# Kernel optimization log

Hardware: AMD Instinct MI355X
Metric: run time of the kernel (lower is better)

Reference implementation:

```python
import jax, jax.numpy as jnp
import numpy as np

D, L, G, B, T = 512, 2, 64, 64, 512  # n_dim, n_layers, n_gaussian, batch, seq_len


def lstm_cell(x, h, c, Wih, Whh, bih, bhh):
    # PyTorch gate order: input, forget, cell(g), output
    g = x @ Wih.T + bih + h @ Whh.T + bhh  # [B, 4D]
    i, f, gg, o = jnp.split(g, 4, axis=-1)
    c = jax.nn.sigmoid(f) * c + jax.nn.sigmoid(i) * jnp.tanh(gg)
    h = jax.nn.sigmoid(o) * jnp.tanh(c)
    return h, c


def encode(x, Wih, Whh, bih, bhh):
    n = x.shape[0]
    xt = jnp.transpose(x, (1, 0, 2))  # [T, B, D]
    hs, cs = [], []
    for l in range(L):
        def step(carry, xv, l=l):
            h, c = carry
            h, c = lstm_cell(xv, h, c, Wih[l], Whh[l], bih[l], bhh[l])
            return (h, c), h
        z = jnp.zeros((n, D), x.dtype)
        (hT, cT), xt = jax.lax.scan(step, (z, z), xt)
        hs.append(hT); cs.append(cT)
    return jnp.stack(hs), jnp.stack(cs)  # [L, B, D] each


def decode(prev0, h0, c0, Wih, Whh, bih, bhh, length):
    def step(carry, _):
        prev, h, c = carry
        x = prev
        nh, nc = [], []
        for l in range(L):
            hl, cl = lstm_cell(x, h[l], c[l], Wih[l], Whh[l], bih[l], bhh[l])
            nh.append(hl); nc.append(cl); x = hl
        return (x, jnp.stack(nh), jnp.stack(nc)), x
    _, ys = jax.lax.scan(step, (prev0, h0, c0), None, length=length)
    return jnp.transpose(ys, (1, 0, 2))  # [B, T, D]


def vae(h, muW, mub, sigW, sigb, outW, outb, eps):
    mu = jnp.einsum('lbd,lgd->lbg', h, muW) + mub[:, None, :]
    sig = jnp.einsum('lbd,lgd->lbg', h, sigW) + sigb[:, None, :]
    z = mu + eps * sig  # reparameterization
    out = jnp.einsum('lbg,ldg->lbd', z, outW) + outb[:, None, :]
    return out, mu, sig


def setup_inputs() -> dict:
    key = jax.random.key(0)
    ks = jax.random.split(key, 26)
    kk = 1.0 / np.sqrt(D)
    u = lambda i, shp: jax.random.uniform(ks[i], shp, jnp.float32, -kk, kk)
    return {
        "x": jax.random.normal(ks[0], (B, T, D), jnp.float32),
        "initial": jnp.zeros((1, D), jnp.float32),
        "enc_Wih": u(1, (L, 4 * D, D)), "enc_Whh": u(2, (L, 4 * D, D)),
        "enc_bih": u(3, (L, 4 * D)), "enc_bhh": u(4, (L, 4 * D)),
        "dec_Wih": u(5, (L, 4 * D, D)), "dec_Whh": u(6, (L, 4 * D, D)),
        "dec_bih": u(7, (L, 4 * D)), "dec_bhh": u(8, (L, 4 * D)),
        "h_mu_W": u(9, (L, G, D)), "h_mu_b": u(10, (L, G)),
        "h_sig_W": u(11, (L, G, D)), "h_sig_b": u(12, (L, G)),
        "h_out_W": u(13, (L, D, G)), "h_out_b": u(14, (L, D)),
        "c_mu_W": u(15, (L, G, D)), "c_mu_b": u(16, (L, G)),
        "c_sig_W": u(17, (L, G, D)), "c_sig_b": u(18, (L, G)),
        "c_out_W": u(19, (L, D, G)), "c_out_b": u(20, (L, D)),
        "eps_h": jax.random.normal(ks[21], (L, B, G), jnp.float32),
        "eps_c": jax.random.normal(ks[22], (L, B, G), jnp.float32),
    }


def reference(x, initial, enc_Wih, enc_Whh, enc_bih, enc_bhh,
              dec_Wih, dec_Whh, dec_bih, dec_bhh,
              h_mu_W, h_mu_b, h_sig_W, h_sig_b, h_out_W, h_out_b,
              c_mu_W, c_mu_b, c_sig_W, c_sig_b, c_out_W, c_out_b,
              eps_h, eps_c):
    h, c = encode(x, enc_Wih, enc_Whh, enc_bih, enc_bhh)
    h2, hmu, hsig = vae(h, h_mu_W, h_mu_b, h_sig_W, h_sig_b, h_out_W, h_out_b, eps_h)
    c2, cmu, csig = vae(c, c_mu_W, c_mu_b, c_sig_W, c_sig_b, c_out_W, c_out_b, eps_c)
    prev0 = jnp.broadcast_to(initial, (x.shape[0], D))
    out = decode(prev0, h2, c2, dec_Wih, dec_Whh, dec_bih, dec_bhh, x.shape[1])
    return out, jnp.concatenate([hmu, cmu], 0), jnp.concatenate([hsig, csig], 0)
```

## Files before the change

### kernel.cpp

```cpp
#include <hip/hip_runtime.h>
#include <hip/hip_bf16.h>

typedef __bf16 bf16_t;
typedef __attribute__((ext_vector_type(8))) __bf16 bf16x8;
typedef __attribute__((ext_vector_type(4))) float f32x4;
typedef __attribute__((ext_vector_type(4))) int i32x4;

#define MFMA16(a, b, c) __builtin_amdgcn_mfma_f32_16x16x32_bf16((a), (b), (c), 0, 0, 0)

namespace {
constexpr int TSEQ = 512, DDIM = 512, NB = 64;
constexpr size_t OFF_ENC_HBUF = 0;
constexpr size_t OFF_DEC_HBUF = 262144;
constexpr size_t OFF_DEC_YBUF = 524288;
constexpr size_t OFF_HT       = 655360;
constexpr size_t OFF_CT       = 917504;
constexpr size_t OFF_H2       = 1179648;
constexpr size_t OFF_C2       = 1441792;
constexpr size_t OFF_GX       = 2097152;
constexpr size_t GX_BYTES     = (size_t)512 * 256 * 256 * 4;
constexpr int RETRY_CAP = 1 << 14;
template <int V> struct IC { static constexpr int v = V; };
}

__device__ __forceinline__ float sigm_f(float x) { return 1.f / (1.f + __expf(-x)); }
__device__ __forceinline__ float tanh_f(float x) {
  x = fminf(15.f, fmaxf(-15.f, x));
  const float e = __expf(-2.f * x);
  return (1.f - e) / (1.f + e);
}
__device__ __forceinline__ bf16x8 cvt8(const float* __restrict__ p) {
  const float4 a = *(const float4*)p;
  const float4 b = *(const float4*)(p + 4);
  bf16x8 r;
  r[0] = (bf16_t)a.x; r[1] = (bf16_t)a.y; r[2] = (bf16_t)a.z; r[3] = (bf16_t)a.w;
  r[4] = (bf16_t)b.x; r[5] = (bf16_t)b.y; r[6] = (bf16_t)b.z; r[7] = (bf16_t)b.w;
  return r;
}

union FRAG { i32x4 i; bf16x8 v; };

__device__ __forceinline__ unsigned tagpat(int g) {
  return ((((g + 1) >> 1) & 1) ^ 1) ? 0x00010001u : 0u;
}
__device__ __forceinline__ unsigned chk4(const i32x4& v, unsigned pat) {
  unsigned bad = 0;
#pragma unroll
  for (int j = 0; j < 4; ++j) bad |= ((unsigned)v[j] ^ pat) & 0x00010001u;
  return bad;
}

__device__ __forceinline__ void ldg_issue(const bf16_t* p, i32x4& d) {
  asm volatile("global_load_dwordx4 %0, %1, off sc1" : "=v"(d) : "v"(p) : "memory");
}
__device__ __forceinline__ void vm_wait0() {
  asm volatile("s_waitcnt vmcnt(0)" ::: "memory");
  __builtin_amdgcn_sched_barrier(0);
}
__device__ __forceinline__ void stg_tag(bf16_t* p, float a, float b, unsigned pat) {
  union { bf16_t h[2]; unsigned u; } x;
  x.h[0] = (bf16_t)a; x.h[1] = (bf16_t)b;
  __hip_atomic_store((unsigned*)p, (x.u & ~0x00010001u) | pat,
                     __ATOMIC_RELAXED, __HIP_MEMORY_SCOPE_AGENT);
}

__device__ __forceinline__ void load_weights(const float* Wih, const float* Whh,
                                             int wave, int c15, int kg, int d0,
                                             bf16x8 (&wA)[2][8], bf16x8 (&wB)[2][8]) {
  const float* Wsrc = (wave < 2) ? Wih : Whh;
  const int kb = (wave & 1) << 8;
#pragma unroll
  for (int l = 0; l < 2; ++l)
#pragma unroll
    for (int nt = 0; nt < 2; ++nt)
#pragma unroll
      for (int ks = 0; ks < 8; ++ks) {
        const int n = nt * 16 + c15;
        const int grow = (n >> 3) * DDIM + d0 + (n & 7);
        const float* p = Wsrc + (size_t)(l * 2048 + grow) * DDIM + kb + ks * 32 + kg * 8;
        if (nt == 0) wA[l][ks] = cvt8(p);
        else         wB[l][ks] = cvt8(p);
      }
}

__global__ __launch_bounds__(256, 4) void gx_pass(
    const float* __restrict__ x, const float* __restrict__ Wih,
    unsigned* __restrict__ gx) {
  const int wg0 = blockIdx.x & 255;
  const int tc  = blockIdx.x >> 8;
  const int grp = wg0 >> 6, slc = wg0 & 63;
  const int tid = threadIdx.x;
  const int wave = tid >> 6, lane = tid & 63;
  const int c15 = lane & 15, kg = lane >> 4;
  const int b0 = grp << 4, d0 = slc << 3;
  const int kb = (wave & 1) << 8;
  const int tpar = wave >> 1;

  __shared__ float gbuf[2][2][16][33];

  bf16x8 wA[8], wB[8];
#pragma unroll
  for (int nt = 0; nt < 2; ++nt)
#pragma unroll
    for (int ks = 0; ks < 8; ++ks) {
      const int n = nt * 16 + c15;
      const int grow = (n >> 3) * DDIM + d0 + (n & 7);
      const float* p = Wih + (size_t)grow * DDIM + kb + ks * 32 + kg * 8;
      if (nt == 0) wA[ks] = cvt8(p);
      else         wB[ks] = cvt8(p);
    }

  const int b = b0 + c15;
  for (int j = 0; j < 32; ++j) {
    const int t = tc * 64 + 2 * j + tpar;
    f32x4 a0 = {0.f, 0.f, 0.f, 0.f}, a1 = {0.f, 0.f, 0.f, 0.f};
    const float* ap = x + ((size_t)b * TSEQ + t) * DDIM + kb + kg * 8;
#pragma unroll
    for (int ks = 0; ks < 8; ++ks) {
      const bf16x8 a = cvt8(ap + ks * 32);
      a0 = MFMA16(a, wA[ks], a0);
      a1 = MFMA16(a, wB[ks], a1);
    }
#pragma unroll
    for (int r = 0; r < 4; ++r) {
      gbuf[tpar][wave & 1][kg * 4 + r][c15] = a0[r];
      gbuf[tpar][wave & 1][kg * 4 + r][16 + c15] = a1[r];
    }
    __syncthreads();
    if (tid < 128) {
      const int ll = tid >> 6, r6 = tid & 63, rw = r6 >> 2, dp = r6 & 3;
      const int tt = tc * 64 + 2 * j + ll;
      const size_t base = ((size_t)tt * 256 + wg0) * 256 + rw * 16 + dp;
#pragma unroll
      for (int g = 0; g < 4; ++g) {
        const int e = g * 8 + 2 * dp;
        const float v0 = gbuf[ll][0][rw][e] + gbuf[ll][1][rw][e];
        const float v1 = gbuf[ll][0][rw][e + 1] + gbuf[ll][1][rw][e + 1];
        union { _Float16 h[2]; unsigned u; } pk;
        pk.h[0] = (_Float16)v0; pk.h[1] = (_Float16)v1;
        __builtin_nontemporal_store(pk.u, &gx[base + g * 4]);
      }
    }
    __syncthreads();
  }
}

template <int GX>
__global__ __launch_bounds__(256, 1) void enc_pass(
    const float* __restrict__ x,
    const float* __restrict__ Wih, const float* __restrict__ Whh,
    const float* __restrict__ bih, const float* __restrict__ bhh,
    bf16_t* __restrict__ hbuf, float* __restrict__ hT, float* __restrict__ cT,
    const unsigned* __restrict__ gx) {
  const int wg = blockIdx.x;
  const int grp = wg >> 6, slc = wg & 63;
  const int tid = threadIdx.x;
  const int wave = tid >> 6, lane = tid & 63;
  const int b0 = grp << 4, d0 = slc << 3;

  __shared__ float gbuf[2][4][16][33];
  __shared__ float bias_l[2][32];

  const int c15 = lane & 15, kg = lane >> 4;
  const int b = b0 + c15;

  bf16x8 wA[2][8], wB[2][8];
  load_weights(Wih, Whh, wave, c15, kg, d0, wA, wB);
  if (tid < 64) {
    const int l = tid >> 5, n = tid & 31;
    const int grow = (n >> 3) * DDIM + d0 + (n & 7);
    bias_l[l][n] = bih[l * 2048 + grow] + bhh[l * 2048 + grow];
  }
  if (tid < 128) {
    const int l = tid >> 6, r6 = tid & 63, rw = r6 >> 2, dp = r6 & 3;
    const int slot = (l == 0) ? 1 : 0;
    stg_tag(&hbuf[((size_t)(l * 2 + slot) * NB + b0 + rw) * DDIM + d0 + 2 * dp],
            0.f, 0.f, 0x00010001u);
  }
  __syncthreads();

  float cA = 0.f, cB = 0.f;

  for (int s = 0; s <= TSEQ; ++s) {
    const int p = s & 1, rp = p ^ 1;
    const unsigned patold = tagpat(s - 1);
    f32x4 pa0 = {0.f, 0.f, 0.f, 0.f}, pa1 = {0.f, 0.f, 0.f, 0.f};
    unsigned gxr[4];
    if constexpr (GX) {
      if (tid < 64 && s < TSEQ) {
        const size_t base = ((size_t)s * 256 + wg) * 256 + (tid >> 2) * 16 + (tid & 3);
#pragma unroll
        for (int g = 0; g < 4; ++g) gxr[g] = __builtin_nontemporal_load(&gx[base + g * 4]);
      }
    } else {
      if (wave < 2 && s < TSEQ) {
        const int kq = wave << 8;
        const float* ap = x + ((size_t)b * TSEQ + s) * DDIM + kq + kg * 8;
#pragma unroll
        for (int ks = 0; ks < 8; ++ks) {
          const bf16x8 a = cvt8(ap + ks * 32);
          pa0 = MFMA16(a, wA[0][ks], pa0);
          pa1 = MFMA16(a, wB[0][ks], pa1);
        }
      }
    }
    __syncthreads();
    if (wave >= 2) {
      const int kq = (wave - 2) << 8;
      FRAG f0[8], f1[8];
      const bf16_t* a0p = hbuf + ((size_t)(0 * 2 + rp) * NB + b) * DDIM + kq + kg * 8;
      const bf16_t* a1p = hbuf + ((size_t)(1 * 2 + rp) * NB + b) * DDIM + kq + kg * 8;
      int guard = 0;
      for (;;) {
        if (s < TSEQ) {
#pragma unroll
          for (int ks = 0; ks < 8; ++ks) ldg_issue(a0p + ks * 32, f0[ks].i);
        }
        if (s >= 1) {
#pragma unroll
          for (int ks = 0; ks < 8; ++ks) ldg_issue(a1p + ks * 32, f1[ks].i);
        }
        vm_wait0();
        unsigned bad = 0;
        if (s < TSEQ) {
#pragma unroll
          for (int ks = 0; ks < 8; ++ks) bad |= chk4(f0[ks].i, patold);
        }
        if (s >= 1) {
#pragma unroll
          for (int ks = 0; ks < 8; ++ks) bad |= chk4(f1[ks].i, patold);
        }
        if (__all(bad == 0) || ++guard > RETRY_CAP) break;
      }
      if (s < TSEQ) {
        f32x4 a0 = {0.f, 0.f, 0.f, 0.f}, a1 = {0.f, 0.f, 0.f, 0.f};
#pragma unroll
        for (int ks = 0; ks < 8; ++ks) {
          a0 = MFMA16(f0[ks].v, wA[0][ks], a0);
          a1 = MFMA16(f0[ks].v, wB[0][ks], a1);
        }
#pragma unroll
        for (int r = 0; r < 4; ++r) {
          gbuf[0][wave][kg * 4 + r][c15] = a0[r];
          gbuf[0][wave][kg * 4 + r][16 + c15] = a1[r];
        }
      }
      if (s >= 1) {
        f32x4 a0 = {0.f, 0.f, 0.f, 0.f}, a1 = {0.f, 0.f, 0.f, 0.f};
#pragma unroll
        for (int ks = 0; ks < 8; ++ks) {
          a0 = MFMA16(f1[ks].v, wA[1][ks], a0);
          a1 = MFMA16(f1[ks].v, wB[1][ks], a1);
        }
#pragma unroll
        for (int r = 0; r < 4; ++r) {
          gbuf[1][wave][kg * 4 + r][c15] = a0[r];
          gbuf[1][wave][kg * 4 + r][16 + c15] = a1[r];
        }
      }
    } else {
      if constexpr (!GX) {
        if (s < TSEQ) {
#pragma unroll
          for (int r = 0; r < 4; ++r) {
            gbuf[0][wave][kg * 4 + r][c15] = pa0[r];
            gbuf[0][wave][kg * 4 + r][16 + c15] = pa1[r];
          }
        }
      }
      if (s >= 1) {
        const int kq = wave << 8;
        FRAG f[8];
        const bf16_t* ap = hbuf + ((size_t)(0 * 2 + rp) * NB + b) * DDIM + kq + kg * 8;
        int guard = 0;
        for (;;) {
#pragma unroll
          for (int ks = 0; ks < 8; ++ks) ldg_issue(ap + ks * 32, f[ks].i);
          vm_wait0();
          unsigned bad = 0;
#pragma unroll
          for (int ks = 0; ks < 8; ++ks) bad |= chk4(f[ks].i, patold);
          if (__all(bad == 0) || ++guard > RETRY_CAP) break;
        }
        f32x4 a0 = {0.f, 0.f, 0.f, 0.f}, a1 = {0.f, 0.f, 0.f, 0.f};
#pragma unroll
        for (int ks = 0; ks < 8; ++ks) {
          a0 = MFMA16(f[ks].v, wA[1][ks], a0);
          a1 = MFMA16(f[ks].v, wB[1][ks], a1);
        }
#pragma unroll
        for (int r = 0; r < 4; ++r) {
          gbuf[1][wave][kg * 4 + r][c15] = a0[r];
          gbuf[1][wave][kg * 4 + r][16 + c15] = a1[r];
        }
      }
    }
    __syncthreads();
    if (tid < 128) {
      const int ll = tid >> 6, r6 = tid & 63, rw = r6 >> 2, dp = r6 & 3;
      const bool act = (ll == 0) ? (s < TSEQ) : (s >= 1);
      if (act) {
        const unsigned pat = tagpat(s);
        float gs[4][2];
#pragma unroll
        for (int g = 0; g < 4; ++g) {
          gs[g][0] = bias_l[ll][g * 8 + 2 * dp];
          gs[g][1] = bias_l[ll][g * 8 + 2 * dp + 1];
        }
        if (GX && ll == 0) {
#pragma unroll
          for (int g = 0; g < 4; ++g) {
            union { unsigned u; _Float16 h[2]; } dk;
            dk.u = gxr[g];
            gs[g][0] += (float)dk.h[0];
            gs[g][1] += (float)dk.h[1];
          }
        }
        const int q0 = (GX && ll == 0) ? 2 : 0;
#pragma unroll
        for (int q = 0; q < 4; ++q) {
          if (q >= q0) {
#pragma unroll
            for (int g = 0; g < 4; ++g) {
              const int e = g * 8 + 2 * dp;
              gs[g][0] += gbuf[ll][q][rw][e];
              gs[g][1] += gbuf[ll][q][rw][e + 1];
            }
          }
        }
        float hv2[2], cv2[2];
#pragma unroll
        for (int e2 = 0; e2 < 2; ++e2) {
          const float iv = sigm_f(gs[0][e2]), fv = sigm_f(gs[1][e2]);
          const float gv = tanh_f(gs[2][e2]), ov = sigm_f(gs[3][e2]);
          float& cs = (e2 == 0) ? cA : cB;
          cs = fv * cs + iv * gv;
          cv2[e2] = cs;
          hv2[e2] = ov * tanh_f(cs);
        }
        const int b2 = b0 + rw, dc = d0 + dp * 2;
        stg_tag(&hbuf[((size_t)(ll * 2 + p) * NB + b2) * DDIM + dc], hv2[0], hv2[1], pat);
        if ((ll == 0 && s == TSEQ - 1) || (ll == 1 && s == TSEQ)) {
          *(float2*)&hT[((size_t)ll * NB + b2) * DDIM + dc] = float2{hv2[0], hv2[1]};
          *(float2*)&cT[((size_t)ll * NB + b2) * DDIM + dc] = float2{cv2[0], cv2[1]};
        }
      }
    }
  }
}

__global__ __launch_bounds__(256, 1) void dec_pass(
    const float* __restrict__ initial,
    const float* __restrict__ Wih, const float* __restrict__ Whh,
    const float* __restrict__ bih, const float* __restrict__ bhh,
    const float* __restrict__ h_init, const float* __restrict__ c_init,
    bf16_t* __restrict__ hbuf, bf16_t* __restrict__ ybuf,
    float* __restrict__ out) {
  const int wg = blockIdx.x;
  const int grp = wg >> 6, slc = wg & 63;
  const int tid = threadIdx.x;
  const int wave = tid >> 6, lane = tid & 63;
  const int b0 = grp << 4, d0 = slc << 3;

  __shared__ float gbuf[4][16][33];
  __shared__ float bias_l[2][32];

  const int c15 = lane & 15, kg = lane >> 4;
  const int b = b0 + c15;

  bf16x8 wA[2][8], wB[2][8];
  load_weights(Wih, Whh, wave, c15, kg, d0, wA, wB);
  if (tid < 64) {
    const int l = tid >> 5, n = tid & 31;
    const int grow = (n >> 3) * DDIM + d0 + (n & 7);
    bias_l[l][n] = bih[l * 2048 + grow] + bhh[l * 2048 + grow];
  }
  if (tid < 128) {
    const int l = tid >> 6, r6 = tid & 63, rw = r6 >> 2, dp = r6 & 3;
    const int b2 = b0 + rw, dc = d0 + 2 * dp;
    const float2 hv = *(const float2*)&h_init[((size_t)l * NB + b2) * DDIM + dc];
    stg_tag(&hbuf[((size_t)(l * 2 + 1) * NB + b2) * DDIM + dc], hv.x, hv.y, 0x00010001u);
  }
  if (tid < 64) {
    const int rw = tid >> 2, dp = tid & 3;
    const int dc = d0 + 2 * dp;
    stg_tag(&ybuf[((size_t)1 * NB + b0 + rw) * DDIM + dc], initial[dc], initial[dc + 1],
            0x00010001u);
  }
  const int rw0 = lane >> 2, dp0 = lane & 3;
  float cA0 = 0.f, cB0 = 0.f, cA1 = 0.f, cB1 = 0.f;
  if (wave == 0) {
    const float2 c0 = *(const float2*)&c_init[((size_t)0 * NB + b0 + rw0) * DDIM + d0 + 2 * dp0];
    const float2 c1 = *(const float2*)&c_init[((size_t)1 * NB + b0 + rw0) * DDIM + d0 + 2 * dp0];
    cA0 = c0.x; cB0 = c0.y; cA1 = c1.x; cB1 = c1.y;
  }
  __syncthreads();

  auto level = [&](auto lcc, const int t, const int p, const int rp) {
    constexpr int LC = decltype(lcc)::v;
    const unsigned patold = tagpat(t - 1);
    f32x4 pa0 = {0.f, 0.f, 0.f, 0.f}, pa1 = {0.f, 0.f, 0.f, 0.f};
    if (wave >= 2) {
      const int kq = (wave - 2) << 8;
      FRAG f[8];
      const bf16_t* ap = hbuf + ((size_t)(LC * 2 + rp) * NB + b) * DDIM + kq + kg * 8;
      int guard = 0;
      for (;;) {
#pragma unroll
        for (int ks = 0; ks < 8; ++ks) ldg_issue(ap + ks * 32, f[ks].i);
        vm_wait0();
        unsigned bad = 0;
#pragma unroll
        for (int ks = 0; ks < 8; ++ks) bad |= chk4(f[ks].i, patold);
        if (__all(bad == 0) || ++guard > RETRY_CAP) break;
      }
#pragma unroll
      for (int ks = 0; ks < 8; ++ks) {
        pa0 = MFMA16(f[ks].v, wA[LC][ks], pa0);
        pa1 = MFMA16(f[ks].v, wB[LC][ks], pa1);
      }
    }
    __syncthreads();
    if (wave >= 2) {
#pragma unroll
      for (int r = 0; r < 4; ++r) {
        gbuf[wave][kg * 4 + r][c15] = pa0[r];
        gbuf[wave][kg * 4 + r][16 + c15] = pa1[r];
      }
    } else {
      const int kq = wave << 8;
      const unsigned patf = (LC == 0) ? patold : tagpat(t);
      const bf16_t* base = (LC == 0) ? (ybuf + (size_t)rp * NB * DDIM)
                                     : (hbuf + (size_t)(0 * 2 + p) * NB * DDIM);
      const bf16_t* ap = base + (size_t)b * DDIM + kq + kg * 8;
      FRAG f[8];
      int guard = 0;
      for (;;) {
#pragma unroll
        for (int ks = 0; ks < 8; ++ks) ldg_issue(ap + ks * 32, f[ks].i);
        vm_wait0();
        unsigned bad = 0;
#pragma unroll
        for (int ks = 0; ks < 8; ++ks) bad |= chk4(f[ks].i, patf);
        if (__all(bad == 0) || ++guard > RETRY_CAP) break;
      }
      f32x4 a0 = {0.f, 0.f, 0.f, 0.f}, a1 = {0.f, 0.f, 0.f, 0.f};
#pragma unroll
      for (int ks = 0; ks < 8; ++ks) {
        a0 = MFMA16(f[ks].v, wA[LC][ks], a0);
        a1 = MFMA16(f[ks].v, wB[LC][ks], a1);
      }
#pragma unroll
      for (int r = 0; r < 4; ++r) {
        gbuf[wave][kg * 4 + r][c15] = a0[r];
        gbuf[wave][kg * 4 + r][16 + c15] = a1[r];
      }
    }
    __syncthreads();
    if (tid < 64) {
      const unsigned pat = tagpat(t);
      float hv2[2];
#pragma unroll
      for (int e2 = 0; e2 < 2; ++e2) {
        const int e = dp0 * 2 + e2;
        float gi = bias_l[LC][e],      gf = bias_l[LC][8 + e];
        float gg = bias_l[LC][16 + e], go = bias_l[LC][24 + e];
#pragma unroll
        for (int q = 0; q < 4; ++q) {
          gi += gbuf[q][rw0][e];
          gf += gbuf[q][rw0][8 + e];
          gg += gbuf[q][rw0][16 + e];
          go += gbuf[q][rw0][24 + e];
        }
        const float iv = sigm_f(gi), fv = sigm_f(gf), gv = tanh_f(gg), ov = sigm_f(go);
        float& cs = (LC == 0) ? ((e2 == 0) ? cA0 : cB0) : ((e2 == 0) ? cA1 : cB1);
        cs = fv * cs + iv * gv;
        hv2[e2] = ov * tanh_f(cs);
      }
      const int b2 = b0 + rw0, dc = d0 + dp0 * 2;
      stg_tag(&hbuf[((size_t)(LC * 2 + p) * NB + b2) * DDIM + dc], hv2[0], hv2[1], pat);
      if (LC == 1) {
        stg_tag(&ybuf[((size_t)p * NB + b2) * DDIM + dc], hv2[0], hv2[1], pat);
        union { float f[2]; unsigned long long u; } ov;
        ov.f[0] = hv2[0]; ov.f[1] = hv2[1];
        __builtin_nontemporal_store(ov.u, (unsigned long long*)&out[((size_t)b2 * TSEQ + t) * DDIM + dc]);
      }
    }
  };

  for (int t = 0; t < TSEQ; ++t) {
    const int p = t & 1, rp = p ^ 1;
    level(IC<0>{}, t, p, rp);
    level(IC<1>{}, t, p, rp);
  }
}

__global__ __launch_bounds__(512) void vae_kernel(
    const float* __restrict__ hT, const float* __restrict__ cT,
    const float* __restrict__ hmuW, const float* __restrict__ hmub,
    const float* __restrict__ hsigW, const float* __restrict__ hsigb,
    const float* __restrict__ houtW, const float* __restrict__ houtb,
    const float* __restrict__ cmuW, const float* __restrict__ cmub,
    const float* __restrict__ csigW, const float* __restrict__ csigb,
    const float* __restrict__ coutW, const float* __restrict__ coutb,
    const float* __restrict__ eps_h, const float* __restrict__ eps_c,
    float* __restrict__ h2, float* __restrict__ c2, float* __restrict__ out) {
  const int bid = blockIdx.x;
  const int b = bid & 63;
  const int l = (bid >> 6) & 1;
  const int hc = bid >> 7;
  const int tid = threadIdx.x;

  const float* S    = (hc ? cT : hT) + (l * 64 + b) * 512;
  const float* muW  = (hc ? cmuW : hmuW) + l * 64 * 512;
  const float* mub  = (hc ? cmub : hmub) + l * 64;
  const float* sigW = (hc ? csigW : hsigW) + l * 64 * 512;
  const float* sigb = (hc ? csigb : hsigb) + l * 64;
  const float* outW = (hc ? coutW : houtW) + l * 512 * 64;
  const float* outb = (hc ? coutb : houtb) + l * 512;
  const float* eps  = (hc ? eps_c : eps_h) + (l * 64 + b) * 64;
  float* S2 = (hc ? c2 : h2) + (l * 64 + b) * 512;

  __shared__ float srow[512];
  __shared__ float z[64];
  srow[tid] = S[tid];
  __syncthreads();
  if (tid < 64) {
    const float* wm = muW + tid * 512;
    const float* ws = sigW + tid * 512;
    float mu = mub[tid], sg = sigb[tid];
    for (int d = 0; d < 512; ++d) {
      mu = fmaf(srow[d], wm[d], mu);
      sg = fmaf(srow[d], ws[d], sg);
    }
    z[tid] = mu + eps[tid] * sg;
    const size_t base = (size_t)64 * 512 * 512;
    const size_t idx = ((size_t)(hc * 2 + l) * 64 + b) * 64 + tid;
    out[base + idx] = mu;
    out[base + 4 * 64 * 64 + idx] = sg;
  }
  __syncthreads();
  {
    const float* wo = outW + tid * 64;
    float acc = outb[tid];
#pragma unroll 8
    for (int g = 0; g < 64; ++g) acc = fmaf(z[g], wo[g], acc);
    S2[tid] = acc;
  }
}

extern "C" void kernel_launch(void* const* d_in, const int* in_sizes, int n_in,
                              void* d_out, int out_size, void* d_ws, size_t ws_size,
                              hipStream_t stream) {
  const float* x       = (const float*)d_in[0];
  const float* initial = (const float*)d_in[1];
  const float* eWih    = (const float*)d_in[2];
  const float* eWhh    = (const float*)d_in[3];
  const float* ebih    = (const float*)d_in[4];
  const float* ebhh    = (const float*)d_in[5];
  const float* dWih    = (const float*)d_in[6];
  const float* dWhh    = (const float*)d_in[7];
  const float* dbih    = (const float*)d_in[8];
  const float* dbhh    = (const float*)d_in[9];
  const float* hmuW    = (const float*)d_in[10];
  const float* hmub    = (const float*)d_in[11];
  const float* hsigW   = (const float*)d_in[12];
  const float* hsigb   = (const float*)d_in[13];
  const float* houtW   = (const float*)d_in[14];
  const float* houtb   = (const float*)d_in[15];
  const float* cmuW    = (const float*)d_in[16];
  const float* cmub    = (const float*)d_in[17];
  const float* csigW   = (const float*)d_in[18];
  const float* csigb   = (const float*)d_in[19];
  const float* coutW   = (const float*)d_in[20];
  const float* coutb   = (const float*)d_in[21];
  const float* eps_h   = (const float*)d_in[22];
  const float* eps_c   = (const float*)d_in[23];

  char* ws = (char*)d_ws;
  bf16_t* enc_hbuf = (bf16_t*)(ws + OFF_ENC_HBUF);
  bf16_t* dec_hbuf = (bf16_t*)(ws + OFF_DEC_HBUF);
  bf16_t* dec_ybuf = (bf16_t*)(ws + OFF_DEC_YBUF);
  float* hT = (float*)(ws + OFF_HT);
  float* cT = (float*)(ws + OFF_CT);
  float* h2 = (float*)(ws + OFF_H2);
  float* c2 = (float*)(ws + OFF_C2);
  unsigned* gx = (unsigned*)(ws + OFF_GX);
  float* out = (float*)d_out;

  hipMemsetAsync(ws, 0, OFF_HT, stream);

  const bool use_gx = (ws_size >= OFF_GX + GX_BYTES);
  if (use_gx) {
    gx_pass<<<2048, 256, 0, stream>>>(x, eWih, gx);
    enc_pass<1><<<256, 256, 0, stream>>>(x, eWih, eWhh, ebih, ebhh, enc_hbuf, hT, cT, gx);
  } else {
    enc_pass<0><<<256, 256, 0, stream>>>(x, eWih, eWhh, ebih, ebhh, enc_hbuf, hT, cT, nullptr);
  }
  vae_kernel<<<256, 512, 0, stream>>>(hT, cT, hmuW, hmub, hsigW, hsigb, houtW, houtb,
                                      cmuW, cmub, csigW, csigb, coutW, coutb,
                                      eps_h, eps_c, h2, c2, out);
  dec_pass<<<256, 256, 0, stream>>>(initial, dWih, dWhh, dbih, dbhh,
                                    h2, c2, dec_hbuf, dec_ybuf, out);
}
```

Baseline: 4.890 ms.

## Repartition LSTM recurrence into 128 workgroups of 512 threads with 16-wide slices

Each persistent workgroup now owns 16 hidden columns instead of 8 and runs 8 waves, with each wave covering a 128-wide K slice instead of 256, and the grid shrinks from 256 to 128 blocks in the encoder, decoder and gx precompute. Fewer workgroups take part in the tag-polled global synchronisation each step, and each wave's per-step MFMA chain and load count are halved. The cost is more per-block LDS reduction (8 partials), more register weight storage per wave, and only half the CUs in use, so the recurrence-limited step latency is what decides the outcome.

```diff
diff --git a/kernel.cpp b/kernel.cpp
--- a/kernel.cpp
+++ b/kernel.cpp
@@ -18,7 +18,7 @@
 constexpr size_t OFF_H2       = 1179648;
 constexpr size_t OFF_C2       = 1441792;
 constexpr size_t OFF_GX       = 2097152;
-constexpr size_t GX_BYTES     = (size_t)512 * 256 * 256 * 4;
+constexpr size_t GX_BYTES     = (size_t)512 * 128 * 512 * 4;
 constexpr int RETRY_CAP = 1 << 14;
 template <int V> struct IC { static constexpr int v = V; };
 }
@@ -64,81 +64,59 @@
                      __ATOMIC_RELAXED, __HIP_MEMORY_SCOPE_AGENT);
 }
 
-__device__ __forceinline__ void load_weights(const float* Wih, const float* Whh,
-                                             int wave, int c15, int kg, int d0,
-                                             bf16x8 (&wA)[2][8], bf16x8 (&wB)[2][8]) {
-  const float* Wsrc = (wave < 2) ? Wih : Whh;
-  const int kb = (wave & 1) << 8;
-#pragma unroll
-  for (int l = 0; l < 2; ++l)
-#pragma unroll
-    for (int nt = 0; nt < 2; ++nt)
-#pragma unroll
-      for (int ks = 0; ks < 8; ++ks) {
-        const int n = nt * 16 + c15;
-        const int grow = (n >> 3) * DDIM + d0 + (n & 7);
-        const float* p = Wsrc + (size_t)(l * 2048 + grow) * DDIM + kb + ks * 32 + kg * 8;
-        if (nt == 0) wA[l][ks] = cvt8(p);
-        else         wB[l][ks] = cvt8(p);
-      }
-}
-
 __global__ __launch_bounds__(256, 4) void gx_pass(
     const float* __restrict__ x, const float* __restrict__ Wih,
     unsigned* __restrict__ gx) {
-  const int wg0 = blockIdx.x & 255;
-  const int tc  = blockIdx.x >> 8;
-  const int grp = wg0 >> 6, slc = wg0 & 63;
+  const int wg0 = blockIdx.x & 127;
+  const int tc  = blockIdx.x >> 7;
+  const int grp = wg0 >> 5, slc = wg0 & 31;
   const int tid = threadIdx.x;
-  const int wave = tid >> 6, lane = tid & 63;
+  const int w = tid >> 6, lane = tid & 63;
   const int c15 = lane & 15, kg = lane >> 4;
-  const int b0 = grp << 4, d0 = slc << 3;
-  const int kb = (wave & 1) << 8;
-  const int tpar = wave >> 1;
-
-  __shared__ float gbuf[2][2][16][33];
-
-  bf16x8 wA[8], wB[8];
-#pragma unroll
-  for (int nt = 0; nt < 2; ++nt)
-#pragma unroll
-    for (int ks = 0; ks < 8; ++ks) {
-      const int n = nt * 16 + c15;
-      const int grow = (n >> 3) * DDIM + d0 + (n & 7);
-      const float* p = Wih + (size_t)grow * DDIM + kb + ks * 32 + kg * 8;
-      if (nt == 0) wA[ks] = cvt8(p);
-      else         wB[ks] = cvt8(p);
-    }
+  const int b0 = grp << 4, d0 = slc << 4;
+  const int kb = w << 7;
+
+  __shared__ float gbuf[4][16][68];
+
+  bf16x8 wX[4][4];
+#pragma unroll
+  for (int nt = 0; nt < 4; ++nt)
+#pragma unroll
+    for (int ks = 0; ks < 4; ++ks)
+      wX[nt][ks] = cvt8(Wih + (size_t)(nt * DDIM + d0 + c15) * DDIM + kb + ks * 32 + kg * 8);
 
   const int b = b0 + c15;
-  for (int j = 0; j < 32; ++j) {
-    const int t = tc * 64 + 2 * j + tpar;
-    f32x4 a0 = {0.f, 0.f, 0.f, 0.f}, a1 = {0.f, 0.f, 0.f, 0.f};
+  for (int j = 0; j < 64; ++j) {
+    const int t = tc * 64 + j;
+    f32x4 acc[4];
+#pragma unroll
+    for (int nt = 0; nt < 4; ++nt) acc[nt] = f32x4{0.f, 0.f, 0.f, 0.f};
     const float* ap = x + ((size_t)b * TSEQ + t) * DDIM + kb + kg * 8;
 #pragma unroll
-    for (int ks = 0; ks < 8; ++ks) {
+    for (int ks = 0; ks < 4; ++ks) {
       const bf16x8 a = cvt8(ap + ks * 32);
-      a0 = MFMA16(a, wA[ks], a0);
-      a1 = MFMA16(a, wB[ks], a1);
-    }
-#pragma unroll
-    for (int r = 0; r < 4; ++r) {
-      gbuf[tpar][wave & 1][kg * 4 + r][c15] = a0[r];
-      gbuf[tpar][wave & 1][kg * 4 + r][16 + c15] = a1[r];
-    }
+#pragma unroll
+      for (int nt = 0; nt < 4; ++nt) acc[nt] = MFMA16(a, wX[nt][ks], acc[nt]);
+    }
+#pragma unroll
+    for (int nt = 0; nt < 4; ++nt)
+#pragma unroll
+      for (int r = 0; r < 4; ++r) gbuf[w][kg * 4 + r][nt * 16 + c15] = acc[nt][r];
     __syncthreads();
     if (tid < 128) {
-      const int ll = tid >> 6, r6 = tid & 63, rw = r6 >> 2, dp = r6 & 3;
-      const int tt = tc * 64 + 2 * j + ll;
-      const size_t base = ((size_t)tt * 256 + wg0) * 256 + rw * 16 + dp;
+      const int rw = tid >> 3, dp = tid & 7;
+      const size_t base = ((size_t)t * 128 + wg0) * 512 + rw * 32;
 #pragma unroll
       for (int g = 0; g < 4; ++g) {
-        const int e = g * 8 + 2 * dp;
-        const float v0 = gbuf[ll][0][rw][e] + gbuf[ll][1][rw][e];
-        const float v1 = gbuf[ll][0][rw][e + 1] + gbuf[ll][1][rw][e + 1];
+        float v0 = 0.f, v1 = 0.f;
+#pragma unroll
+        for (int q = 0; q < 4; ++q) {
+          const float2 v = *(const float2*)&gbuf[q][rw][g * 16 + 2 * dp];
+          v0 += v.x; v1 += v.y;
+        }
         union { _Float16 h[2]; unsigned u; } pk;
         pk.h[0] = (_Float16)v0; pk.h[1] = (_Float16)v1;
-        __builtin_nontemporal_store(pk.u, &gx[base + g * 4]);
+        __builtin_nontemporal_store(pk.u, &gx[base + g * 8 + dp]);
       }
     }
     __syncthreads();
@@ -146,168 +124,189 @@
 }
 
 template <int GX>
-__global__ __launch_bounds__(256, 1) void enc_pass(
+__global__ __launch_bounds__(512, 1) void enc_pass(
     const float* __restrict__ x,
     const float* __restrict__ Wih, const float* __restrict__ Whh,
     const float* __restrict__ bih, const float* __restrict__ bhh,
     bf16_t* __restrict__ hbuf, float* __restrict__ hT, float* __restrict__ cT,
     const unsigned* __restrict__ gx) {
   const int wg = blockIdx.x;
-  const int grp = wg >> 6, slc = wg & 63;
+  const int grp = wg >> 5, slc = wg & 31;
   const int tid = threadIdx.x;
-  const int wave = tid >> 6, lane = tid & 63;
-  const int b0 = grp << 4, d0 = slc << 3;
-
-  __shared__ float gbuf[2][4][16][33];
-  __shared__ float bias_l[2][32];
-
+  const int w = tid >> 6, lane = tid & 63;
   const int c15 = lane & 15, kg = lane >> 4;
+  const int b0 = grp << 4, d0 = slc << 4;
+  const int kb = (w & 3) << 7;
   const int b = b0 + c15;
 
-  bf16x8 wA[2][8], wB[2][8];
-  load_weights(Wih, Whh, wave, c15, kg, d0, wA, wB);
-  if (tid < 64) {
-    const int l = tid >> 5, n = tid & 31;
-    const int grow = (n >> 3) * DDIM + d0 + (n & 7);
+  __shared__ float gbuf[2][8][16][68];
+  __shared__ float bias_l[2][64];
+
+  bf16x8 wI[4][4];
+  bf16x8 wR[2][4][4];
+  bf16x8 wX[4][4];
+  if (w < 4) {
+#pragma unroll
+    for (int nt = 0; nt < 4; ++nt)
+#pragma unroll
+      for (int ks = 0; ks < 4; ++ks)
+        wI[nt][ks] = cvt8(Wih + (size_t)(2048 + nt * DDIM + d0 + c15) * DDIM + kb + ks * 32 + kg * 8);
+    if (!GX) {
+#pragma unroll
+      for (int nt = 0; nt < 4; ++nt)
+#pragma unroll
+        for (int ks = 0; ks < 4; ++ks)
+          wX[nt][ks] = cvt8(Wih + (size_t)(nt * DDIM + d0 + c15) * DDIM + kb + ks * 32 + kg * 8);
+    }
+  } else {
+#pragma unroll
+    for (int l = 0; l < 2; ++l)
+#pragma unroll
+      for (int nt = 0; nt < 4; ++nt)
+#pragma unroll
+        for (int ks = 0; ks < 4; ++ks)
+          wR[l][nt][ks] = cvt8(Whh + (size_t)(l * 2048 + nt * DDIM + d0 + c15) * DDIM + kb + ks * 32 + kg * 8);
+  }
+  if (tid < 128) {
+    const int l = tid >> 6, n = tid & 63;
+    const int grow = (n >> 4) * DDIM + d0 + (n & 15);
     bias_l[l][n] = bih[l * 2048 + grow] + bhh[l * 2048 + grow];
   }
-  if (tid < 128) {
-    const int l = tid >> 6, r6 = tid & 63, rw = r6 >> 2, dp = r6 & 3;
+  if (tid < 256) {
+    const int l = tid >> 7, r6 = tid & 127, rw = r6 >> 3, dpp = r6 & 7;
     const int slot = (l == 0) ? 1 : 0;
-    stg_tag(&hbuf[((size_t)(l * 2 + slot) * NB + b0 + rw) * DDIM + d0 + 2 * dp],
+    stg_tag(&hbuf[((size_t)(l * 2 + slot) * NB + b0 + rw) * DDIM + d0 + 2 * dpp],
             0.f, 0.f, 0x00010001u);
   }
   __syncthreads();
 
+  const int ell = tid >> 7, erw = (tid & 127) >> 3, edp = tid & 7;
   float cA = 0.f, cB = 0.f;
 
   for (int s = 0; s <= TSEQ; ++s) {
     const int p = s & 1, rp = p ^ 1;
     const unsigned patold = tagpat(s - 1);
-    f32x4 pa0 = {0.f, 0.f, 0.f, 0.f}, pa1 = {0.f, 0.f, 0.f, 0.f};
     unsigned gxr[4];
+    f32x4 px[4];
     if constexpr (GX) {
-      if (tid < 64 && s < TSEQ) {
-        const size_t base = ((size_t)s * 256 + wg) * 256 + (tid >> 2) * 16 + (tid & 3);
-#pragma unroll
-        for (int g = 0; g < 4; ++g) gxr[g] = __builtin_nontemporal_load(&gx[base + g * 4]);
+      if (tid < 128 && s < TSEQ) {
+        const size_t base = ((size_t)s * 128 + wg) * 512 + erw * 32;
+#pragma unroll
+        for (int g = 0; g < 4; ++g) gxr[g] = __builtin_nontemporal_load(&gx[base + g * 8 + edp]);
       }
     } else {
-      if (wave < 2 && s < TSEQ) {
-        const int kq = wave << 8;
-        const float* ap = x + ((size_t)b * TSEQ + s) * DDIM + kq + kg * 8;
-#pragma unroll
-        for (int ks = 0; ks < 8; ++ks) {
+      if (w < 4 && s < TSEQ) {
+#pragma unroll
+        for (int nt = 0; nt < 4; ++nt) px[nt] = f32x4{0.f, 0.f, 0.f, 0.f};
+        const float* ap = x + ((size_t)b * TSEQ + s) * DDIM + kb + kg * 8;
+#pragma unroll
+        for (int ks = 0; ks < 4; ++ks) {
           const bf16x8 a = cvt8(ap + ks * 32);
-          pa0 = MFMA16(a, wA[0][ks], pa0);
-          pa1 = MFMA16(a, wB[0][ks], pa1);
+#pragma unroll
+          for (int nt = 0; nt < 4; ++nt) px[nt] = MFMA16(a, wX[nt][ks], px[nt]);
         }
       }
     }
     __syncthreads();
-    if (wave >= 2) {
-      const int kq = (wave - 2) << 8;
-      FRAG f0[8], f1[8];
-      const bf16_t* a0p = hbuf + ((size_t)(0 * 2 + rp) * NB + b) * DDIM + kq + kg * 8;
-      const bf16_t* a1p = hbuf + ((size_t)(1 * 2 + rp) * NB + b) * DDIM + kq + kg * 8;
+    if (w >= 4) {
+      FRAG f0[4], f1[4];
+      const bf16_t* a0p = hbuf + ((size_t)(0 * 2 + rp) * NB + b) * DDIM + kb + kg * 8;
+      const bf16_t* a1p = hbuf + ((size_t)(1 * 2 + rp) * NB + b) * DDIM + kb + kg * 8;
       int guard = 0;
       for (;;) {
         if (s < TSEQ) {
 #pragma unroll
-          for (int ks = 0; ks < 8; ++ks) ldg_issue(a0p + ks * 32, f0[ks].i);
+          for (int ks = 0; ks < 4; ++ks) ldg_issue(a0p + ks * 32, f0[ks].i);
         }
         if (s >= 1) {
 #pragma unroll
-          for (int ks = 0; ks < 8; ++ks) ldg_issue(a1p + ks * 32, f1[ks].i);
+          for (int ks = 0; ks < 4; ++ks) ldg_issue(a1p + ks * 32, f1[ks].i);
         }
         vm_wait0();
         unsigned bad = 0;
         if (s < TSEQ) {
 #pragma unroll
-          for (int ks = 0; ks < 8; ++ks) bad |= chk4(f0[ks].i, patold);
+          for (int ks = 0; ks < 4; ++ks) bad |= chk4(f0[ks].i, patold);
         }
         if (s >= 1) {
 #pragma unroll
-          for (int ks = 0; ks < 8; ++ks) bad |= chk4(f1[ks].i, patold);
+          for (int ks = 0; ks < 4; ++ks) bad |= chk4(f1[ks].i, patold);
         }
         if (__all(bad == 0) || ++guard > RETRY_CAP) break;
       }
       if (s < TSEQ) {
-        f32x4 a0 = {0.f, 0.f, 0.f, 0.f}, a1 = {0.f, 0.f, 0.f, 0.f};
-#pragma unroll
-        for (int ks = 0; ks < 8; ++ks) {
-          a0 = MFMA16(f0[ks].v, wA[0][ks], a0);
-          a1 = MFMA16(f0[ks].v, wB[0][ks], a1);
-        }
-#pragma unroll
-        for (int r = 0; r < 4; ++r) {
-          gbuf[0][wave][kg * 4 + r][c15] = a0[r];
-          gbuf[0][wave][kg * 4 + r][16 + c15] = a1[r];
-        }
+        f32x4 acc[4];
+#pragma unroll
+        for (int nt = 0; nt < 4; ++nt) acc[nt] = f32x4{0.f, 0.f, 0.f, 0.f};
+#pragma unroll
+        for (int ks = 0; ks < 4; ++ks)
+#pragma unroll
+          for (int nt = 0; nt < 4; ++nt) acc[nt] = MFMA16(f0[ks].v, wR[0][nt][ks], acc[nt]);
+#pragma unroll
+        for (int nt = 0; nt < 4; ++nt)
+#pragma unroll
+          for (int r = 0; r < 4; ++r) gbuf[0][w][kg * 4 + r][nt * 16 + c15] = acc[nt][r];
       }
       if (s >= 1) {
-        f32x4 a0 = {0.f, 0.f, 0.f, 0.f}, a1 = {0.f, 0.f, 0.f, 0.f};
-#pragma unroll
-        for (int ks = 0; ks < 8; ++ks) {
-          a0 = MFMA16(f1[ks].v, wA[1][ks], a0);
-          a1 = MFMA16(f1[ks].v, wB[1][ks], a1);
-        }
-#pragma unroll
-        for (int r = 0; r < 4; ++r) {
-          gbuf[1][wave][kg * 4 + r][c15] = a0[r];
-          gbuf[1][wave][kg * 4 + r][16 + c15] = a1[r];
-        }
+        f32x4 acc[4];
+#pragma unroll
+        for (int nt = 0; nt < 4; ++nt) acc[nt] = f32x4{0.f, 0.f, 0.f, 0.f};
+#pragma unroll
+        for (int ks = 0; ks < 4; ++ks)
+#pragma unroll
+          for (int nt = 0; nt < 4; ++nt) acc[nt] = MFMA16(f1[ks].v, wR[1][nt][ks], acc[nt]);
+#pragma unroll
+        for (int nt = 0; nt < 4; ++nt)
+#pragma unroll
+          for (int r = 0; r < 4; ++r) gbuf[1][w][kg * 4 + r][nt * 16 + c15] = acc[nt][r];
       }
     } else {
       if constexpr (!GX) {
         if (s < TSEQ) {
 #pragma unroll
-          for (int r = 0; r < 4; ++r) {
-            gbuf[0][wave][kg * 4 + r][c15] = pa0[r];
-            gbuf[0][wave][kg * 4 + r][16 + c15] = pa1[r];
-          }
+          for (int nt = 0; nt < 4; ++nt)
+#pragma unroll
+            for (int r = 0; r < 4; ++r) gbuf[0][w][kg * 4 + r][nt * 16 + c15] = px[nt][r];
         }
       }
       if (s >= 1) {
-        const int kq = wave << 8;
-        FRAG f[8];
-        const bf16_t* ap = hbuf + ((size_t)(0 * 2 + rp) * NB + b) * DDIM + kq + kg * 8;
+        FRAG f[4];
+        const bf16_t* ap = hbuf + ((size_t)(0 * 2 + rp) * NB + b) * DDIM + kb + kg * 8;
         int guard = 0;
         for (;;) {
 #pragma unroll
-          for (int ks = 0; ks < 8; ++ks) ldg_issue(ap + ks * 32, f[ks].i);
+          for (int ks = 0; ks < 4; ++ks) ldg_issue(ap + ks * 32, f[ks].i);
           vm_wait0();
           unsigned bad = 0;
 #pragma unroll
-          for (int ks = 0; ks < 8; ++ks) bad |= chk4(f[ks].i, patold);
+          for (int ks = 0; ks < 4; ++ks) bad |= chk4(f[ks].i, patold);
           if (__all(bad == 0) || ++guard > RETRY_CAP) break;
         }
-        f32x4 a0 = {0.f, 0.f, 0.f, 0.f}, a1 = {0.f, 0.f, 0.f, 0.f};
-#pragma unroll
-        for (int ks = 0; ks < 8; ++ks) {
-          a0 = MFMA16(f[ks].v, wA[1][ks], a0);
-          a1 = MFMA16(f[ks].v, wB[1][ks], a1);
-        }
-#pragma unroll
-        for (int r = 0; r < 4; ++r) {
-          gbuf[1][wave][kg * 4 + r][c15] = a0[r];
-          gbuf[1][wave][kg * 4 + r][16 + c15] = a1[r];
-        }
+        f32x4 acc[4];
+#pragma unroll
+        for (int nt = 0; nt < 4; ++nt) acc[nt] = f32x4{0.f, 0.f, 0.f, 0.f};
+#pragma unroll
+        for (int ks = 0; ks < 4; ++ks)
+#pragma unroll
+          for (int nt = 0; nt < 4; ++nt) acc[nt] = MFMA16(f[ks].v, wI[nt][ks], acc[nt]);
+#pragma unroll
+        for (int nt = 0; nt < 4; ++nt)
+#pragma unroll
+          for (int r = 0; r < 4; ++r) gbuf[1][w][kg * 4 + r][nt * 16 + c15] = acc[nt][r];
       }
     }
     __syncthreads();
-    if (tid < 128) {
-      const int ll = tid >> 6, r6 = tid & 63, rw = r6 >> 2, dp = r6 & 3;
-      const bool act = (ll == 0) ? (s < TSEQ) : (s >= 1);
+    if (tid < 256) {
+      const bool act = (ell == 0) ? (s < TSEQ) : (s >= 1);
       if (act) {
         const unsigned pat = tagpat(s);
         float gs[4][2];
 #pragma unroll
         for (int g = 0; g < 4; ++g) {
-          gs[g][0] = bias_l[ll][g * 8 + 2 * dp];
-          gs[g][1] = bias_l[ll][g * 8 + 2 * dp + 1];
-        }
-        if (GX && ll == 0) {
+          gs[g][0] = bias_l[ell][g * 16 + 2 * edp];
+          gs[g][1] = bias_l[ell][g * 16 + 2 * edp + 1];
+        }
+        if (GX && ell == 0) {
 #pragma unroll
           for (int g = 0; g < 4; ++g) {
             union { unsigned u; _Float16 h[2]; } dk;
@@ -316,15 +315,14 @@
             gs[g][1] += (float)dk.h[1];
           }
         }
-        const int q0 = (GX && ll == 0) ? 2 : 0;
-#pragma unroll
-        for (int q = 0; q < 4; ++q) {
+        const int q0 = (GX && ell == 0) ? 4 : 0;
+#pragma unroll
+        for (int q = 0; q < 8; ++q) {
           if (q >= q0) {
 #pragma unroll
             for (int g = 0; g < 4; ++g) {
-              const int e = g * 8 + 2 * dp;
-              gs[g][0] += gbuf[ll][q][rw][e];
-              gs[g][1] += gbuf[ll][q][rw][e + 1];
+              const float2 v = *(const float2*)&gbuf[ell][q][erw][g * 16 + 2 * edp];
+              gs[g][0] += v.x; gs[g][1] += v.y;
             }
           }
         }
@@ -333,23 +331,23 @@
         for (int e2 = 0; e2 < 2; ++e2) {
           const float iv = sigm_f(gs[0][e2]), fv = sigm_f(gs[1][e2]);
           const float gv = tanh_f(gs[2][e2]), ov = sigm_f(gs[3][e2]);
-          float& cs = (e2 == 0) ? cA : cB;
-          cs = fv * cs + iv * gv;
-          cv2[e2] = cs;
-          hv2[e2] = ov * tanh_f(cs);
-        }
-        const int b2 = b0 + rw, dc = d0 + dp * 2;
-        stg_tag(&hbuf[((size_t)(ll * 2 + p) * NB + b2) * DDIM + dc], hv2[0], hv2[1], pat);
-        if ((ll == 0 && s == TSEQ - 1) || (ll == 1 && s == TSEQ)) {
-          *(float2*)&hT[((size_t)ll * NB + b2) * DDIM + dc] = float2{hv2[0], hv2[1]};
-          *(float2*)&cT[((size_t)ll * NB + b2) * DDIM + dc] = float2{cv2[0], cv2[1]};
-        }
-      }
-    }
-  }
-}
-
-__global__ __launch_bounds__(256, 1) void dec_pass(
+          float& cst = (e2 == 0) ? cA : cB;
+          cst = fv * cst + iv * gv;
+          cv2[e2] = cst;
+          hv2[e2] = ov * tanh_f(cst);
+        }
+        const int b2 = b0 + erw, dc = d0 + 2 * edp;
+        stg_tag(&hbuf[((size_t)(ell * 2 + p) * NB + b2) * DDIM + dc], hv2[0], hv2[1], pat);
+        if ((ell == 0 && s == TSEQ - 1) || (ell == 1 && s == TSEQ)) {
+          *(float2*)&hT[((size_t)ell * NB + b2) * DDIM + dc] = float2{hv2[0], hv2[1]};
+          *(float2*)&cT[((size_t)ell * NB + b2) * DDIM + dc] = float2{cv2[0], cv2[1]};
+        }
+      }
+    }
+  }
+}
+
+__global__ __launch_bounds__(512, 1) void dec_pass(
     const float* __restrict__ initial,
     const float* __restrict__ Wih, const float* __restrict__ Whh,
     const float* __restrict__ bih, const float* __restrict__ bhh,
@@ -357,127 +355,138 @@
     bf16_t* __restrict__ hbuf, bf16_t* __restrict__ ybuf,
     float* __restrict__ out) {
   const int wg = blockIdx.x;
-  const int grp = wg >> 6, slc = wg & 63;
+  const int grp = wg >> 5, slc = wg & 31;
   const int tid = threadIdx.x;
-  const int wave = tid >> 6, lane = tid & 63;
-  const int b0 = grp << 4, d0 = slc << 3;
-
-  __shared__ float gbuf[4][16][33];
-  __shared__ float bias_l[2][32];
-
+  const int w = tid >> 6, lane = tid & 63;
   const int c15 = lane & 15, kg = lane >> 4;
+  const int b0 = grp << 4, d0 = slc << 4;
+  const int kb = (w & 3) << 7;
   const int b = b0 + c15;
 
-  bf16x8 wA[2][8], wB[2][8];
-  load_weights(Wih, Whh, wave, c15, kg, d0, wA, wB);
-  if (tid < 64) {
-    const int l = tid >> 5, n = tid & 31;
-    const int grow = (n >> 3) * DDIM + d0 + (n & 7);
+  __shared__ float gbuf[8][16][68];
+  __shared__ float bias_l[2][64];
+
+  bf16x8 wF[2][4][4];
+  {
+    const float* Wsrc = (w < 4) ? Wih : Whh;
+#pragma unroll
+    for (int l = 0; l < 2; ++l)
+#pragma unroll
+      for (int nt = 0; nt < 4; ++nt)
+#pragma unroll
+        for (int ks = 0; ks < 4; ++ks)
+          wF[l][nt][ks] = cvt8(Wsrc + (size_t)(l * 2048 + nt * DDIM + d0 + c15) * DDIM + kb + ks * 32 + kg * 8);
+  }
+  if (tid < 128) {
+    const int l = tid >> 6, n = tid & 63;
+    const int grow = (n >> 4) * DDIM + d0 + (n & 15);
     bias_l[l][n] = bih[l * 2048 + grow] + bhh[l * 2048 + grow];
   }
-  if (tid < 128) {
-    const int l = tid >> 6, r6 = tid & 63, rw = r6 >> 2, dp = r6 & 3;
-    const int b2 = b0 + rw, dc = d0 + 2 * dp;
+  if (tid < 256) {
+    const int l = tid >> 7, r6 = tid & 127, rw = r6 >> 3, dpp = r6 & 7;
+    const int b2 = b0 + rw, dc = d0 + 2 * dpp;
     const float2 hv = *(const float2*)&h_init[((size_t)l * NB + b2) * DDIM + dc];
     stg_tag(&hbuf[((size_t)(l * 2 + 1) * NB + b2) * DDIM + dc], hv.x, hv.y, 0x00010001u);
   }
-  if (tid < 64) {
-    const int rw = tid >> 2, dp = tid & 3;
-    const int dc = d0 + 2 * dp;
+  if (tid < 128) {
+    const int rw = tid >> 3, dpp = tid & 7;
+    const int dc = d0 + 2 * dpp;
     stg_tag(&ybuf[((size_t)1 * NB + b0 + rw) * DDIM + dc], initial[dc], initial[dc + 1],
             0x00010001u);
   }
-  const int rw0 = lane >> 2, dp0 = lane & 3;
-  float cA0 = 0.f, cB0 = 0.f, cA1 = 0.f, cB1 = 0.f;
-  if (wave == 0) {
-    const float2 c0 = *(const float2*)&c_init[((size_t)0 * NB + b0 + rw0) * DDIM + d0 + 2 * dp0];
-    const float2 c1 = *(const float2*)&c_init[((size_t)1 * NB + b0 + rw0) * DDIM + d0 + 2 * dp0];
-    cA0 = c0.x; cB0 = c0.y; cA1 = c1.x; cB1 = c1.y;
+  const int erw = tid >> 3, edp = tid & 7;
+  float cs[2][2] = {{0.f, 0.f}, {0.f, 0.f}};
+  if (tid < 128) {
+    const float2 c0 = *(const float2*)&c_init[((size_t)0 * NB + b0 + erw) * DDIM + d0 + 2 * edp];
+    const float2 c1 = *(const float2*)&c_init[((size_t)1 * NB + b0 + erw) * DDIM + d0 + 2 * edp];
+    cs[0][0] = c0.x; cs[0][1] = c0.y; cs[1][0] = c1.x; cs[1][1] = c1.y;
   }
   __syncthreads();
 
   auto level = [&](auto lcc, const int t, const int p, const int rp) {
     constexpr int LC = decltype(lcc)::v;
     const unsigned patold = tagpat(t - 1);
-    f32x4 pa0 = {0.f, 0.f, 0.f, 0.f}, pa1 = {0.f, 0.f, 0.f, 0.f};
-    if (wave >= 2) {
-      const int kq = (wave - 2) << 8;
-      FRAG f[8];
-      const bf16_t* ap = hbuf + ((size_t)(LC * 2 + rp) * NB + b) * DDIM + kq + kg * 8;
+    f32x4 pa[4];
+    if (w >= 4) {
+      FRAG f[4];
+      const bf16_t* ap = hbuf + ((size_t)(LC * 2 + rp) * NB + b) * DDIM + kb + kg * 8;
       int guard = 0;
       for (;;) {
 #pragma unroll
-        for (int ks = 0; ks < 8; ++ks) ldg_issue(ap + ks * 32, f[ks].i);
+        for (int ks = 0; ks < 4; ++ks) ldg_issue(ap + ks * 32, f[ks].i);
         vm_wait0();
         unsigned bad = 0;
 #pragma unroll
-        for (int ks = 0; ks < 8; ++ks) bad |= chk4(f[ks].i, patold);
+        for (int ks = 0; ks < 4; ++ks) bad |= chk4(f[ks].i, patold);
         if (__all(bad == 0) || ++guard > RETRY_CAP) break;
       }
 #pragma unroll
-      for (int ks = 0; ks < 8; ++ks) {
-        pa0 = MFMA16(f[ks].v, wA[LC][ks], pa0);
-        pa1 = MFMA16(f[ks].v, wB[LC][ks], pa1);
-      }
+      for (int nt = 0; nt < 4; ++nt) pa[nt] = f32x4{0.f, 0.f, 0.f, 0.f};
+#pragma unroll
+      for (int ks = 0; ks < 4; ++ks)
+#pragma unroll
+        for (int nt = 0; nt < 4; ++nt) pa[nt] = MFMA16(f[ks].v, wF[LC][nt][ks], pa[nt]);
     }
     __syncthreads();
-    if (wave >= 2) {
-#pragma unroll
-      for (int r = 0; r < 4; ++r) {
-        gbuf[wave][kg * 4 + r][c15] = pa0[r];
-        gbuf[wave][kg * 4 + r][16 + c15] = pa1[r];
-      }
+    if (w >= 4) {
+#pragma unroll
+      for (int nt = 0; nt < 4; ++nt)
+#pragma unroll
+        for (int r = 0; r < 4; ++r) gbuf[w][kg * 4 + r][nt * 16 + c15] = pa[nt][r];
     } else {
-      const int kq = wave << 8;
       const unsigned patf = (LC == 0) ? patold : tagpat(t);
       const bf16_t* base = (LC == 0) ? (ybuf + (size_t)rp * NB * DDIM)
                                      : (hbuf + (size_t)(0 * 2 + p) * NB * DDIM);
-      const bf16_t* ap = base + (size_t)b * DDIM + kq + kg * 8;
-      FRAG f[8];
+      const bf16_t* ap = base + (size_t)b * DDIM + kb + kg * 8;
+      FRAG f[4];
       int guard = 0;
       for (;;) {
 #pragma unroll
-        for (int ks = 0; ks < 8; ++ks) ldg_issue(ap + ks * 32, f[ks].i);
+        for (int ks = 0; ks < 4; ++ks) ldg_issue(ap + ks * 32, f[ks].i);
         vm_wait0();
         unsigned bad = 0;
 #pragma unroll
-        for (int ks = 0; ks < 8; ++ks) bad |= chk4(f[ks].i, patf);
+        for (int ks = 0; ks < 4; ++ks) bad |= chk4(f[ks].i, patf);
         if (__all(bad == 0) || ++guard > RETRY_CAP) break;
       }
-      f32x4 a0 = {0.f, 0.f, 0.f, 0.f}, a1 = {0.f, 0.f, 0.f, 0.f};
-#pragma unroll
-      for (int ks = 0; ks < 8; ++ks) {
-        a0 = MFMA16(f[ks].v, wA[LC][ks], a0);
-        a1 = MFMA16(f[ks].v, wB[LC][ks], a1);
-      }
-#pragma unroll
-      for (int r = 0; r < 4; ++r) {
-        gbuf[wave][kg * 4 + r][c15] = a0[r];
-        gbuf[wave][kg * 4 + r][16 + c15] = a1[r];
-      }
+      f32x4 acc[4];
+#pragma unroll
+      for (int nt = 0; nt < 4; ++nt) acc[nt] = f32x4{0.f, 0.f, 0.f, 0.f};
+#pragma unroll
+      for (int ks = 0; ks < 4; ++ks)
+#pragma unroll
+        for (int nt = 0; nt < 4; ++nt) acc[nt] = MFMA16(f[ks].v, wF[LC][nt][ks], acc[nt]);
+#pragma unroll
+      for (int nt = 0; nt < 4; ++nt)
+#pragma unroll
+        for (int r = 0; r < 4; ++r) gbuf[w][kg * 4 + r][nt * 16 + c15] = acc[nt][r];
     }
     __syncthreads();
-    if (tid < 64) {
+    if (tid < 128) {
       const unsigned pat = tagpat(t);
+      float gs[4][2];
+#pragma unroll
+      for (int g = 0; g < 4; ++g) {
+        gs[g][0] = bias_l[LC][g * 16 + 2 * edp];
+        gs[g][1] = bias_l[LC][g * 16 + 2 * edp + 1];
+      }
+#pragma unroll
+      for (int q = 0; q < 8; ++q)
+#pragma unroll
+        for (int g = 0; g < 4; ++g) {
+          const float2 v = *(const float2*)&gbuf[q][erw][g * 16 + 2 * edp];
+          gs[g][0] += v.x; gs[g][1] += v.y;
+        }
       float hv2[2];
 #pragma unroll
       for (int e2 = 0; e2 < 2; ++e2) {
-        const int e = dp0 * 2 + e2;
-        float gi = bias_l[LC][e],      gf = bias_l[LC][8 + e];
-        float gg = bias_l[LC][16 + e], go = bias_l[LC][24 + e];
-#pragma unroll
-        for (int q = 0; q < 4; ++q) {
-          gi += gbuf[q][rw0][e];
-          gf += gbuf[q][rw0][8 + e];
-          gg += gbuf[q][rw0][16 + e];
-          go += gbuf[q][rw0][24 + e];
-        }
-        const float iv = sigm_f(gi), fv = sigm_f(gf), gv = tanh_f(gg), ov = sigm_f(go);
-        float& cs = (LC == 0) ? ((e2 == 0) ? cA0 : cB0) : ((e2 == 0) ? cA1 : cB1);
-        cs = fv * cs + iv * gv;
-        hv2[e2] = ov * tanh_f(cs);
-      }
-      const int b2 = b0 + rw0, dc = d0 + dp0 * 2;
+        const float iv = sigm_f(gs[0][e2]), fv = sigm_f(gs[1][e2]);
+        const float gv = tanh_f(gs[2][e2]), ov = sigm_f(gs[3][e2]);
+        float& cst = cs[LC][e2];
+        cst = fv * cst + iv * gv;
+        hv2[e2] = ov * tanh_f(cst);
+      }
+      const int b2 = b0 + erw, dc = d0 + 2 * edp;
       stg_tag(&hbuf[((size_t)(LC * 2 + p) * NB + b2) * DDIM + dc], hv2[0], hv2[1], pat);
       if (LC == 1) {
         stg_tag(&ybuf[((size_t)p * NB + b2) * DDIM + dc], hv2[0], hv2[1], pat);
@@ -592,14 +601,14 @@
 
   const bool use_gx = (ws_size >= OFF_GX + GX_BYTES);
   if (use_gx) {
-    gx_pass<<<2048, 256, 0, stream>>>(x, eWih, gx);
-    enc_pass<1><<<256, 256, 0, stream>>>(x, eWih, eWhh, ebih, ebhh, enc_hbuf, hT, cT, gx);
+    gx_pass<<<1024, 256, 0, stream>>>(x, eWih, gx);
+    enc_pass<1><<<128, 512, 0, stream>>>(x, eWih, eWhh, ebih, ebhh, enc_hbuf, hT, cT, gx);
   } else {
-    enc_pass<0><<<256, 256, 0, stream>>>(x, eWih, eWhh, ebih, ebhh, enc_hbuf, hT, cT, nullptr);
+    enc_pass<0><<<128, 512, 0, stream>>>(x, eWih, eWhh, ebih, ebhh, enc_hbuf, hT, cT, nullptr);
   }
   vae_kernel<<<256, 512, 0, stream>>>(hT, cT, hmuW, hmub, hsigW, hsigb, houtW, houtb,
                                       cmuW, cmub, csigW, csigb, coutW, coutb,
                                       eps_h, eps_c, h2, c2, out);
-  dec_pass<<<256, 256, 0, stream>>>(initial, dWih, dWhh, dbih, dbhh,
+  dec_pass<<<128, 512, 0, stream>>>(initial, dWih, dWhh, dbih, dbhh,
                                     h2, c2, dec_hbuf, dec_ybuf, out);
 }
```

After: 5.606 ms. 14.6% more time.
